# Optimization experiments

Measured on AMD Instinct MI355X. Metric: run time of the kernel, lower is better.

The kernel has to match this reference:

```python
import jax, jax.numpy as jnp
import numpy as np

N_NODES = 100000
N_EDGES = 1600000
IN_C, HID_C, OUT_C = 32, 64, 32


def setup_inputs() -> dict:
    key = jax.random.key(0)
    ks = jax.random.split(key, 9)
    x = jax.random.normal(ks[0], (N_NODES, IN_C), dtype=jnp.float32)
    edge_index = jax.random.randint(ks[1], (2, N_EDGES), 0, N_NODES, dtype=jnp.int64)
    # SAGEConv params: lin_l acts on aggregated neighbors (with bias), lin_r on root (no bias)
    s1 = 1.0 / np.sqrt(IN_C)
    s2 = 1.0 / np.sqrt(HID_C)
    W1_l = jax.random.uniform(ks[2], (HID_C, IN_C), minval=-s1, maxval=s1, dtype=jnp.float32)
    W1_r = jax.random.uniform(ks[3], (HID_C, IN_C), minval=-s1, maxval=s1, dtype=jnp.float32)
    b1 = jax.random.uniform(ks[4], (HID_C,), minval=-s1, maxval=s1, dtype=jnp.float32)
    W2_l = jax.random.uniform(ks[5], (OUT_C, HID_C), minval=-s2, maxval=s2, dtype=jnp.float32)
    W2_r = jax.random.uniform(ks[6], (OUT_C, HID_C), minval=-s2, maxval=s2, dtype=jnp.float32)
    b2 = jax.random.uniform(ks[7], (OUT_C,), minval=-s2, maxval=s2, dtype=jnp.float32)
    return {"x": x, "W1_l": W1_l, "W1_r": W1_r, "b1": b1,
            "W2_l": W2_l, "W2_r": W2_r, "b2": b2, "edge_index": edge_index}


def _sage_conv(x, src, dst, W_l, W_r, b, num_nodes):
    # gather messages from source nodes, mean-aggregate onto destination nodes
    msg = x[src]                                                     # [E, C]
    agg = jax.ops.segment_sum(msg, dst, num_segments=num_nodes)      # [N, C]
    deg = jax.ops.segment_sum(jnp.ones((src.shape[0],), dtype=x.dtype), dst,
                              num_segments=num_nodes)                # [N]
    mean = agg / jnp.maximum(deg, 1.0)[:, None]
    # out = lin_l(mean_neighbors) + lin_r(x_root)
    return mean @ W_l.T + x @ W_r.T + b


def reference(x, W1_l, W1_r, b1, W2_l, W2_r, b2, edge_index):
    src, dst = edge_index[0], edge_index[1]
    h = _sage_conv(x, src, dst, W1_l, W1_r, b1, N_NODES)
    h = jax.nn.relu(h)
    out = _sage_conv(h, src, dst, W2_l, W2_r, b2, N_NODES)
    return out
```

## Files before the change

kernel.cpp:

```cpp
#include <hip/hip_runtime.h>

#define N_NODES 100000
#define N_EDGES 1600000
#define IN_C 32
#define HID_C 64
#define OUT_C 32

#define EPB 4096
#define NBLK ((N_EDGES + EPB - 1) / EPB)
#define BSH 8
#define BKN (1 << BSH)
#define NB ((N_NODES + BKN - 1) / BKN)
#define REG 4608

typedef __attribute__((ext_vector_type(8))) short bf16x8;
typedef __attribute__((ext_vector_type(8))) unsigned short u16x8;
typedef __attribute__((ext_vector_type(4))) float f32x4;

__device__ __forceinline__ unsigned short f2bf(float f) {
    unsigned u = __float_as_uint(f);
    return (unsigned short)((u + 0x7fffu + ((u >> 16) & 1u)) >> 16);
}
__device__ __forceinline__ float bf2f(unsigned short h) {
    return __uint_as_float((unsigned)h << 16);
}

__global__ void cast_w_kernel(const float* __restrict__ w1l,
                              const float* __restrict__ w1r,
                              const float* __restrict__ w2l,
                              const float* __restrict__ w2r,
                              ushort* __restrict__ wb, int* __restrict__ bcnt) {
    for (int i = threadIdx.x; i < NB; i += 256) bcnt[i] = 0;
    for (int i = threadIdx.x; i < 8192; i += 256) {
        float v;
        if (i < 2048) v = w1l[i];
        else if (i < 4096) v = w1r[i - 2048];
        else if (i < 6144) v = w2l[i - 4096];
        else v = w2r[i - 6144];
        wb[i] = f2bf(v);
    }
}

__global__ __launch_bounds__(256) void place_kernel(
    const int* __restrict__ src, const int* __restrict__ dst,
    const float* __restrict__ x, ushort* __restrict__ xbA,
    ushort* __restrict__ xbB, int* __restrict__ bcnt,
    unsigned* __restrict__ tmp) {
    for (int ci = blockIdx.x * 256 + threadIdx.x; ci < N_NODES * IN_C / 8;
         ci += NBLK * 256) {
        int n = ci >> 2;
        int oc = ci & 3;
        const float4* p = (const float4*)&x[(size_t)ci * 8];
        float4 a = p[0], b = p[1];
        u16x8 o;
        o[0] = f2bf(a.x); o[1] = f2bf(a.y); o[2] = f2bf(a.z); o[3] = f2bf(a.w);
        o[4] = f2bf(b.x); o[5] = f2bf(b.y); o[6] = f2bf(b.z); o[7] = f2bf(b.w);
        ushort* dstp = (oc < 2) ? xbA : xbB;
        *(u16x8*)&dstp[(size_t)n * 16 + (oc & 1) * 8] = o;
    }

    __shared__ int lh[NB];
    __shared__ int cur[NB];
    for (int i = threadIdx.x; i < NB; i += 256) lh[i] = 0;
    __syncthreads();

    int base = blockIdx.x * EPB;
    int se[16], de[16];
#pragma unroll
    for (int j = 0; j < 16; ++j) {
        int e = base + j * 256 + threadIdx.x;
        bool v = e < N_EDGES;
        se[j] = v ? src[e] : -1;
        de[j] = v ? dst[e] : 0;
        if (v) atomicAdd(&lh[de[j] >> BSH], 1);
    }
    __syncthreads();
    for (int i = threadIdx.x; i < NB; i += 256)
        cur[i] = i * REG + atomicAdd(&bcnt[i], lh[i]);
    __syncthreads();
#pragma unroll
    for (int j = 0; j < 16; ++j) {
        if (se[j] >= 0) {
            int slot = atomicAdd(&cur[de[j] >> BSH], 1);
            tmp[slot] = ((unsigned)se[j] << 8) | (unsigned)(de[j] & (BKN - 1));
        }
    }
}

__global__ __launch_bounds__(512) void count_place_kernel(
    const unsigned* __restrict__ tmp, const int* __restrict__ bcnt,
    int* __restrict__ counts, int* __restrict__ rowptr,
    int* __restrict__ perm) {
    __shared__ int lcnt[BKN];
    __shared__ int sscan[BKN];
    __shared__ int cur[BKN];
    int b = blockIdx.x;
    int tid = threadIdx.x;
    int start = b * REG;
    int end = start + bcnt[b];

    unsigned pv[9];
    int npv = 0;
    for (int i = start + tid; i < end; i += 512) pv[npv++] = tmp[i];

    if (tid < BKN) lcnt[tid] = 0;
    __syncthreads();
    for (int k = 0; k < npv; ++k)
        atomicAdd(&lcnt[pv[k] & (BKN - 1)], 1);
    __syncthreads();
    if (tid < BKN) sscan[tid] = lcnt[tid];
    __syncthreads();
    for (int o = 1; o < BKN; o <<= 1) {
        int v = 0;
        if (tid < BKN && tid >= o) v = sscan[tid - o];
        __syncthreads();
        if (tid < BKN) sscan[tid] += v;
        __syncthreads();
    }
    if (tid < BKN) {
        int excl = sscan[tid] - lcnt[tid] + start;
        cur[tid] = excl;
        int n = (b << BSH) + tid;
        if (n < N_NODES) { rowptr[n] = excl; counts[n] = lcnt[tid]; }
    }
    __syncthreads();
    for (int k = 0; k < npv; ++k) {
        int slot = atomicAdd(&cur[pv[k] & (BKN - 1)], 1);
        perm[slot] = (int)(pv[k] >> 8);
    }
}

#define GSG8 784

__global__ __launch_bounds__(256) void gather_mean_kernel(
    const ushort* __restrict__ xbA, const ushort* __restrict__ xbB,
    const int* __restrict__ rowptr, const int* __restrict__ counts,
    const int* __restrict__ perm, ushort* __restrict__ mbA,
    ushort* __restrict__ mbB) {
    int g = blockIdx.x;
    int xcd = g & 7;
    int half = xcd >> 2;
    int sub = ((g >> 3) << 2) | (xcd & 3);
    const ushort* xh = half ? xbB : xbA;
    ushort* mh = half ? mbB : mbA;
    int lane = threadIdx.x & 63;
    int wid = threadIdx.x >> 6;
    int n = (sub * 4 + wid) * 32 + (lane >> 1);
    int q = lane & 1;
    if (n >= N_NODES) return;
    int st = rowptr[n];
    int cn = counts[n];

    float acc[8] = {0, 0, 0, 0, 0, 0, 0, 0};
    int i = 0;
    for (; i + 4 <= cn; i += 4) {
        int p0 = perm[st + i + 0];
        int p1 = perm[st + i + 1];
        int p2 = perm[st + i + 2];
        int p3 = perm[st + i + 3];
        u16x8 v0 = *(const u16x8*)&xh[(size_t)p0 * 16 + q * 8];
        u16x8 v1 = *(const u16x8*)&xh[(size_t)p1 * 16 + q * 8];
        u16x8 v2 = *(const u16x8*)&xh[(size_t)p2 * 16 + q * 8];
        u16x8 v3 = *(const u16x8*)&xh[(size_t)p3 * 16 + q * 8];
#pragma unroll
        for (int j = 0; j < 8; ++j)
            acc[j] += (bf2f(v0[j]) + bf2f(v1[j])) + (bf2f(v2[j]) + bf2f(v3[j]));
    }
    for (; i < cn; ++i) {
        int p = perm[st + i];
        u16x8 v = *(const u16x8*)&xh[(size_t)p * 16 + q * 8];
#pragma unroll
        for (int j = 0; j < 8; ++j) acc[j] += bf2f(v[j]);
    }

    float inv = 1.0f / fmaxf((float)cn, 1.0f);
    u16x8 o;
#pragma unroll
    for (int j = 0; j < 8; ++j) o[j] = f2bf(acc[j] * inv);
    *(u16x8*)&mh[(size_t)n * 16 + q * 8] = o;
}

__global__ __launch_bounds__(256) void gather_final_kernel(
    const ushort* __restrict__ tbA, const ushort* __restrict__ tbB,
    const int* __restrict__ rowptr, const int* __restrict__ counts,
    const int* __restrict__ perm, const float* __restrict__ rA,
    const float* __restrict__ rB, float* __restrict__ out) {
    int g = blockIdx.x;
    int xcd = g & 7;
    int half = xcd >> 2;
    int sub = ((g >> 3) << 2) | (xcd & 3);
    const ushort* th = half ? tbB : tbA;
    const float* rh = half ? rB : rA;
    int lane = threadIdx.x & 63;
    int wid = threadIdx.x >> 6;
    int n = (sub * 4 + wid) * 32 + (lane >> 1);
    int q = lane & 1;
    if (n >= N_NODES) return;
    int st = rowptr[n];
    int cn = counts[n];

    float acc[8] = {0, 0, 0, 0, 0, 0, 0, 0};
    int i = 0;
    for (; i + 4 <= cn; i += 4) {
        int p0 = perm[st + i + 0];
        int p1 = perm[st + i + 1];
        int p2 = perm[st + i + 2];
        int p3 = perm[st + i + 3];
        u16x8 v0 = *(const u16x8*)&th[(size_t)p0 * 16 + q * 8];
        u16x8 v1 = *(const u16x8*)&th[(size_t)p1 * 16 + q * 8];
        u16x8 v2 = *(const u16x8*)&th[(size_t)p2 * 16 + q * 8];
        u16x8 v3 = *(const u16x8*)&th[(size_t)p3 * 16 + q * 8];
#pragma unroll
        for (int j = 0; j < 8; ++j)
            acc[j] += (bf2f(v0[j]) + bf2f(v1[j])) + (bf2f(v2[j]) + bf2f(v3[j]));
    }
    for (; i < cn; ++i) {
        int p = perm[st + i];
        u16x8 v = *(const u16x8*)&th[(size_t)p * 16 + q * 8];
#pragma unroll
        for (int j = 0; j < 8; ++j) acc[j] += bf2f(v[j]);
    }

    float inv = 1.0f / fmaxf((float)cn, 1.0f);
    const float4* rp = (const float4*)&rh[(size_t)n * 16 + q * 8];
    float4 r0 = rp[0], r1 = rp[1];
    float4* op = (float4*)&out[(size_t)n * 32 + half * 16 + q * 8];
    op[0] = make_float4(acc[0] * inv + r0.x, acc[1] * inv + r0.y,
                        acc[2] * inv + r0.z, acc[3] * inv + r0.w);
    op[1] = make_float4(acc[4] * inv + r1.x, acc[5] * inv + r1.y,
                        acc[6] * inv + r1.z, acc[7] * inv + r1.w);
}

__global__ __launch_bounds__(256) void transform_mfma_kernel(
    const ushort* __restrict__ xbA, const ushort* __restrict__ xbB,
    const ushort* __restrict__ mbA, const ushort* __restrict__ mbB,
    const ushort* __restrict__ wb, const float* __restrict__ b1,
    const float* __restrict__ b2, ushort* __restrict__ tbA,
    ushort* __restrict__ tbB, float* __restrict__ rA,
    float* __restrict__ rB) {
    __shared__ ushort hlds[4][16 * 72];
    int lane = threadIdx.x & 63;
    int wid = threadIdx.x >> 6;
    int l15 = lane & 15, lhi = lane >> 4;

    const ushort* w1l = wb;
    const ushort* w1r = wb + 2048;
    const ushort* w2l = wb + 4096;
    const ushort* w2r = wb + 6144;

    bf16x8 B1l[4], B1r[4];
#pragma unroll
    for (int jt = 0; jt < 4; ++jt) {
        B1l[jt] = *(const bf16x8*)&w1l[(jt * 16 + l15) * 32 + 8 * lhi];
        B1r[jt] = *(const bf16x8*)&w1r[(jt * 16 + l15) * 32 + 8 * lhi];
    }
    bf16x8 B2l[2][2], B2r[2][2];
#pragma unroll
    for (int ct = 0; ct < 2; ++ct)
#pragma unroll
        for (int kc = 0; kc < 2; ++kc) {
            B2l[ct][kc] = *(const bf16x8*)&w2l[(ct * 16 + l15) * 64 + kc * 32 + 8 * lhi];
            B2r[ct][kc] = *(const bf16x8*)&w2r[(ct * 16 + l15) * 64 + kc * 32 + 8 * lhi];
        }
    float bias1[4];
#pragma unroll
    for (int jt = 0; jt < 4; ++jt) bias1[jt] = b1[jt * 16 + l15];
    float bias2[2] = { b2[l15], b2[16 + l15] };

    ushort* hl = hlds[wid];

#pragma unroll
    for (int chunk = 0; chunk < 2; ++chunk) {
        int n0 = blockIdx.x * 128 + wid * 32 + chunk * 16;
        int nrow = n0 + l15;
        bf16x8 Am = {}, Ax = {};
        if (nrow < N_NODES) {
            const ushort* ms = (lhi < 2) ? mbA : mbB;
            const ushort* xs = (lhi < 2) ? xbA : xbB;
            Am = *(const bf16x8*)&ms[(size_t)nrow * 16 + 8 * (lhi & 1)];
            Ax = *(const bf16x8*)&xs[(size_t)nrow * 16 + 8 * (lhi & 1)];
        }
#pragma unroll
        for (int jt = 0; jt < 4; ++jt) {
            f32x4 acc = {};
            acc = __builtin_amdgcn_mfma_f32_16x16x32_bf16(Am, B1l[jt], acc, 0, 0, 0);
            acc = __builtin_amdgcn_mfma_f32_16x16x32_bf16(Ax, B1r[jt], acc, 0, 0, 0);
#pragma unroll
            for (int reg = 0; reg < 4; ++reg) {
                float h = fmaxf(acc[reg] + bias1[jt], 0.0f);
                hl[(lhi * 4 + reg) * 72 + jt * 16 + l15] = f2bf(h);
            }
        }
        bf16x8 Ah0 = *(const bf16x8*)&hl[l15 * 72 + 8 * lhi];
        bf16x8 Ah1 = *(const bf16x8*)&hl[l15 * 72 + 32 + 8 * lhi];
#pragma unroll
        for (int ct = 0; ct < 2; ++ct) {
            f32x4 acc = {};
            acc = __builtin_amdgcn_mfma_f32_16x16x32_bf16(Ah0, B2l[ct][0], acc, 0, 0, 0);
            acc = __builtin_amdgcn_mfma_f32_16x16x32_bf16(Ah1, B2l[ct][1], acc, 0, 0, 0);
            ushort* tdst = ct ? tbB : tbA;
#pragma unroll
            for (int reg = 0; reg < 4; ++reg) {
                int nr = n0 + lhi * 4 + reg;
                if (nr < N_NODES)
                    tdst[(size_t)nr * 16 + l15] = f2bf(acc[reg]);
            }
        }
#pragma unroll
        for (int ct = 0; ct < 2; ++ct) {
            f32x4 acc = {};
            acc = __builtin_amdgcn_mfma_f32_16x16x32_bf16(Ah0, B2r[ct][0], acc, 0, 0, 0);
            acc = __builtin_amdgcn_mfma_f32_16x16x32_bf16(Ah1, B2r[ct][1], acc, 0, 0, 0);
            float* rdst = ct ? rB : rA;
#pragma unroll
            for (int reg = 0; reg < 4; ++reg) {
                int nr = n0 + lhi * 4 + reg;
                if (nr < N_NODES)
                    rdst[(size_t)nr * 16 + l15] = acc[reg] + bias2[ct];
            }
        }
    }
}


extern "C" void kernel_launch(void* const* d_in, const int* in_sizes, int n_in,
                              void* d_out, int out_size, void* d_ws, size_t ws_size,
                              hipStream_t stream) {
    const float* x   = (const float*)d_in[0];
    const float* W1l = (const float*)d_in[1];
    const float* W1r = (const float*)d_in[2];
    const float* b1  = (const float*)d_in[3];
    const float* W2l = (const float*)d_in[4];
    const float* W2r = (const float*)d_in[5];
    const float* b2  = (const float*)d_in[6];
    const int*   ei  = (const int*)d_in[7];
    const int* src = ei;
    const int* dst = ei + N_EDGES;

    char* ws = (char*)d_ws;
    int*      bcnt   = (int*)ws;             ws += (size_t)(NB + 8) * 4;
    int*      counts = (int*)ws;             ws += (size_t)N_NODES * 4;
    int*      rowptr = (int*)ws;             ws += (size_t)N_NODES * 4;
    int*      perm   = (int*)ws;             ws += (size_t)NB * REG * 4;
    unsigned* tmp    = (unsigned*)ws;        ws += (size_t)NB * REG * 4;
    ushort*   mbA    = (ushort*)tmp;
    ushort*   mbB    = mbA + (size_t)N_NODES * 16;
    ushort*   xbA    = (ushort*)ws;          ws += (size_t)N_NODES * 16 * 2;
    ushort*   xbB    = (ushort*)ws;          ws += (size_t)N_NODES * 16 * 2;
    ushort*   wb     = (ushort*)ws;          ws += (size_t)8192 * 2;
    ushort*   tbA    = (ushort*)ws;          ws += (size_t)N_NODES * 16 * 2;
    ushort*   tbB    = (ushort*)ws;          ws += (size_t)N_NODES * 16 * 2;
    float*    rA     = (float*)ws;           ws += (size_t)N_NODES * 16 * 4;
    float*    rB     = (float*)ws;           ws += (size_t)N_NODES * 16 * 4;

    dim3 blk(256);

    cast_w_kernel<<<1, blk, 0, stream>>>(W1l, W1r, W2l, W2r, wb, bcnt);
    place_kernel<<<NBLK, blk, 0, stream>>>(src, dst, x, xbA, xbB, bcnt, tmp);
    count_place_kernel<<<NB, dim3(512), 0, stream>>>(tmp, bcnt, counts, rowptr, perm);

    gather_mean_kernel<<<2 * GSG8, blk, 0, stream>>>(xbA, xbB, rowptr, counts,
                                                     perm, mbA, mbB);
    transform_mfma_kernel<<<(N_NODES + 127) / 128, blk, 0, stream>>>(
        xbA, xbB, mbA, mbB, wb, b1, b2, tbA, tbB, rA, rB);
    gather_final_kernel<<<2 * GSG8, blk, 0, stream>>>(tbA, tbB, rowptr, counts,
                                                      perm, rA, rB, (float*)d_out);
}
```

Measured before the change: 127.7 us.

## Sort nodes by degree within each bucket to balance gather wavefronts

The count/place kernel now counting-sorts each 256-node bucket's nodes by in-degree (capped at 63) and writes a packed (rowptr|count, node) record into an nsort array in sorted order. Both gather kernels iterate over these sorted slots instead of node ids, so lanes in a wavefront handle nodes of similar degree and diverge less in their loop trip counts. The cost is an extra shared-memory histogram and scan in the placement kernel, an 8-byte indirection load per node, and scattered output writes. The bit packing assumes row offsets fit in 21 bits and counts in 11 bits.

Measured after the change: 144.4 us. 13.0% more time.

```diff
diff --git a/kernel.cpp b/kernel.cpp
--- a/kernel.cpp
+++ b/kernel.cpp
@@ -12,6 +12,7 @@
 #define BKN (1 << BSH)
 #define NB ((N_NODES + BKN - 1) / BKN)
 #define REG 4608
+#define NSLOT (NB * BKN)
 
 typedef __attribute__((ext_vector_type(8))) short bf16x8;
 typedef __attribute__((ext_vector_type(8))) unsigned short u16x8;
@@ -89,11 +90,11 @@
 
 __global__ __launch_bounds__(512) void count_place_kernel(
     const unsigned* __restrict__ tmp, const int* __restrict__ bcnt,
-    int* __restrict__ counts, int* __restrict__ rowptr,
-    int* __restrict__ perm) {
+    uint2* __restrict__ nsort, int* __restrict__ perm) {
     __shared__ int lcnt[BKN];
     __shared__ int sscan[BKN];
     __shared__ int cur[BKN];
+    __shared__ int dbin[64];
     int b = blockIdx.x;
     int tid = threadIdx.x;
     int start = b * REG;
@@ -104,11 +105,18 @@
     for (int i = start + tid; i < end; i += 512) pv[npv++] = tmp[i];
 
     if (tid < BKN) lcnt[tid] = 0;
+    if (tid < 64) dbin[tid] = 0;
     __syncthreads();
     for (int k = 0; k < npv; ++k)
         atomicAdd(&lcnt[pv[k] & (BKN - 1)], 1);
     __syncthreads();
-    if (tid < BKN) sscan[tid] = lcnt[tid];
+    int myc = 0, mybin = 0;
+    if (tid < BKN) {
+        myc = lcnt[tid];
+        mybin = myc < 63 ? myc : 63;
+        sscan[tid] = myc;
+        atomicAdd(&dbin[mybin], 1);
+    }
     __syncthreads();
     for (int o = 1; o < BKN; o <<= 1) {
         int v = 0;
@@ -117,11 +125,22 @@
         if (tid < BKN) sscan[tid] += v;
         __syncthreads();
     }
+    if (tid == 0) {
+        int a = 0;
+#pragma unroll
+        for (int i = 0; i < 64; ++i) { int c = dbin[i]; dbin[i] = a; a += c; }
+    }
+    int excl = 0;
     if (tid < BKN) {
-        int excl = sscan[tid] - lcnt[tid] + start;
+        excl = sscan[tid] - myc + start;
         cur[tid] = excl;
+    }
+    __syncthreads();
+    if (tid < BKN) {
+        int rank = atomicAdd(&dbin[mybin], 1);
         int n = (b << BSH) + tid;
-        if (n < N_NODES) { rowptr[n] = excl; counts[n] = lcnt[tid]; }
+        nsort[(b << BSH) + rank] =
+            make_uint2((unsigned)excl | ((unsigned)myc << 21), (unsigned)n);
     }
     __syncthreads();
     for (int k = 0; k < npv; ++k) {
@@ -134,9 +153,8 @@
 
 __global__ __launch_bounds__(256) void gather_mean_kernel(
     const ushort* __restrict__ xbA, const ushort* __restrict__ xbB,
-    const int* __restrict__ rowptr, const int* __restrict__ counts,
-    const int* __restrict__ perm, ushort* __restrict__ mbA,
-    ushort* __restrict__ mbB) {
+    const uint2* __restrict__ nsort, const int* __restrict__ perm,
+    ushort* __restrict__ mbA, ushort* __restrict__ mbB) {
     int g = blockIdx.x;
     int xcd = g & 7;
     int half = xcd >> 2;
@@ -145,11 +163,13 @@
     ushort* mh = half ? mbB : mbA;
     int lane = threadIdx.x & 63;
     int wid = threadIdx.x >> 6;
-    int n = (sub * 4 + wid) * 32 + (lane >> 1);
+    int slot = (sub * 4 + wid) * 32 + (lane >> 1);
     int q = lane & 1;
-    if (n >= N_NODES) return;
-    int st = rowptr[n];
-    int cn = counts[n];
+    if (slot >= NSLOT) return;
+    uint2 ns = nsort[slot];
+    int st = (int)(ns.x & 0x1FFFFFu);
+    int cn = (int)(ns.x >> 21);
+    int n = (int)ns.y;
 
     float acc[8] = {0, 0, 0, 0, 0, 0, 0, 0};
     int i = 0;
@@ -173,18 +193,20 @@
         for (int j = 0; j < 8; ++j) acc[j] += bf2f(v[j]);
     }
 
-    float inv = 1.0f / fmaxf((float)cn, 1.0f);
-    u16x8 o;
-#pragma unroll
-    for (int j = 0; j < 8; ++j) o[j] = f2bf(acc[j] * inv);
-    *(u16x8*)&mh[(size_t)n * 16 + q * 8] = o;
+    if (n < N_NODES) {
+        float inv = 1.0f / fmaxf((float)cn, 1.0f);
+        u16x8 o;
+#pragma unroll
+        for (int j = 0; j < 8; ++j) o[j] = f2bf(acc[j] * inv);
+        *(u16x8*)&mh[(size_t)n * 16 + q * 8] = o;
+    }
 }
 
 __global__ __launch_bounds__(256) void gather_final_kernel(
     const ushort* __restrict__ tbA, const ushort* __restrict__ tbB,
-    const int* __restrict__ rowptr, const int* __restrict__ counts,
-    const int* __restrict__ perm, const float* __restrict__ rA,
-    const float* __restrict__ rB, float* __restrict__ out) {
+    const uint2* __restrict__ nsort, const int* __restrict__ perm,
+    const float* __restrict__ rA, const float* __restrict__ rB,
+    float* __restrict__ out) {
     int g = blockIdx.x;
     int xcd = g & 7;
     int half = xcd >> 2;
@@ -193,11 +215,13 @@
     const float* rh = half ? rB : rA;
     int lane = threadIdx.x & 63;
     int wid = threadIdx.x >> 6;
-    int n = (sub * 4 + wid) * 32 + (lane >> 1);
+    int slot = (sub * 4 + wid) * 32 + (lane >> 1);
     int q = lane & 1;
-    if (n >= N_NODES) return;
-    int st = rowptr[n];
-    int cn = counts[n];
+    if (slot >= NSLOT) return;
+    uint2 ns = nsort[slot];
+    int st = (int)(ns.x & 0x1FFFFFu);
+    int cn = (int)(ns.x >> 21);
+    int n = (int)ns.y;
 
     float acc[8] = {0, 0, 0, 0, 0, 0, 0, 0};
     int i = 0;
@@ -221,14 +245,16 @@
         for (int j = 0; j < 8; ++j) acc[j] += bf2f(v[j]);
     }
 
-    float inv = 1.0f / fmaxf((float)cn, 1.0f);
-    const float4* rp = (const float4*)&rh[(size_t)n * 16 + q * 8];
-    float4 r0 = rp[0], r1 = rp[1];
-    float4* op = (float4*)&out[(size_t)n * 32 + half * 16 + q * 8];
-    op[0] = make_float4(acc[0] * inv + r0.x, acc[1] * inv + r0.y,
-                        acc[2] * inv + r0.z, acc[3] * inv + r0.w);
-    op[1] = make_float4(acc[4] * inv + r1.x, acc[5] * inv + r1.y,
-                        acc[6] * inv + r1.z, acc[7] * inv + r1.w);
+    if (n < N_NODES) {
+        float inv = 1.0f / fmaxf((float)cn, 1.0f);
+        const float4* rp = (const float4*)&rh[(size_t)n * 16 + q * 8];
+        float4 r0 = rp[0], r1 = rp[1];
+        float4* op = (float4*)&out[(size_t)n * 32 + half * 16 + q * 8];
+        op[0] = make_float4(acc[0] * inv + r0.x, acc[1] * inv + r0.y,
+                            acc[2] * inv + r0.z, acc[3] * inv + r0.w);
+        op[1] = make_float4(acc[4] * inv + r1.x, acc[5] * inv + r1.y,
+                            acc[6] * inv + r1.z, acc[7] * inv + r1.w);
+    }
 }
 
 __global__ __launch_bounds__(256) void transform_mfma_kernel(
@@ -339,8 +365,7 @@
 
     char* ws = (char*)d_ws;
     int*      bcnt   = (int*)ws;             ws += (size_t)(NB + 8) * 4;
-    int*      counts = (int*)ws;             ws += (size_t)N_NODES * 4;
-    int*      rowptr = (int*)ws;             ws += (size_t)N_NODES * 4;
+    uint2*    nsort  = (uint2*)ws;           ws += (size_t)NSLOT * 8;
     int*      perm   = (int*)ws;             ws += (size_t)NB * REG * 4;
     unsigned* tmp    = (unsigned*)ws;        ws += (size_t)NB * REG * 4;
     ushort*   mbA    = (ushort*)tmp;
@@ -357,12 +382,12 @@
 
     cast_w_kernel<<<1, blk, 0, stream>>>(W1l, W1r, W2l, W2r, wb, bcnt);
     place_kernel<<<NBLK, blk, 0, stream>>>(src, dst, x, xbA, xbB, bcnt, tmp);
-    count_place_kernel<<<NB, dim3(512), 0, stream>>>(tmp, bcnt, counts, rowptr, perm);
-
-    gather_mean_kernel<<<2 * GSG8, blk, 0, stream>>>(xbA, xbB, rowptr, counts,
-                                                     perm, mbA, mbB);
+    count_place_kernel<<<NB, dim3(512), 0, stream>>>(tmp, bcnt, nsort, perm);
+
+    gather_mean_kernel<<<2 * GSG8, blk, 0, stream>>>(xbA, xbB, nsort, perm,
+                                                     mbA, mbB);
     transform_mfma_kernel<<<(N_NODES + 127) / 128, blk, 0, stream>>>(
         xbA, xbB, mbA, mbB, wb, b1, b2, tbA, tbB, rA, rB);
-    gather_final_kernel<<<2 * GSG8, blk, 0, stream>>>(tbA, tbB, rowptr, counts,
-                                                      perm, rA, rB, (float*)d_out);
-}
+    gather_final_kernel<<<2 * GSG8, blk, 0, stream>>>(tbA, tbB, nsort, perm,
+                                                      rA, rB, (float*)d_out);
+}
```
